# Performance work log

Hardware: AMD Instinct MI355X
Metric: run time of the kernel (lower is better)

Reference implementation:

```python
import jax, jax.numpy as jnp
import numpy as np

D = 1024        # embedding_dim
H = 16          # num_heads
HKV = 4         # num_kv_heads
HD = D // H     # head_dim = 64
L = 64          # latent_dim
EPS = 1e-6
LN_EPS = 1e-5
B, S = 2, 1024


def _feat(x):
    # feature_map == 'elu': elu(x) + 1 (non-negative features)
    return jax.nn.elu(x) + 1.0


def setup_inputs() -> dict:
    key = jax.random.key(0)
    ks = jax.random.split(key, 8)
    w = lambda k, shape: (jax.random.normal(k, shape, jnp.float32) * 0.02)
    return {
        "x": jax.random.normal(ks[0], (B, S, D), jnp.float32),
        "Wq": w(ks[1], (D, D)), "bq": jnp.zeros((D,), jnp.float32),
        "Wk": w(ks[2], (D, HKV * HD)), "bk": jnp.zeros((HKV * HD,), jnp.float32),
        "Wv": w(ks[3], (D, HKV * HD)), "bv": jnp.zeros((HKV * HD,), jnp.float32),
        "Wc": w(ks[4], (HKV * HD, L)),   # kv_compress (no bias)
        "We": w(ks[5], (L, HKV * HD)),   # kv_expand (no bias)
        "Wo": w(ks[6], (D, D)), "bo": jnp.zeros((D,), jnp.float32),
        "gamma": jnp.ones((D,), jnp.float32),
        "beta": jnp.zeros((D,), jnp.float32),
    }


def reference(x, Wq, bq, Wk, bk, Wv, bv, Wc, We, Wo, bo, gamma, beta):
    b, s, _ = x.shape
    residual = x
    # projections
    q = x @ Wq + bq                     # [b,s,D]
    k = x @ Wk + bk                     # [b,s,HKV*HD]
    v = x @ Wv + bv
    # latent compress -> expand
    k = (k @ Wc) @ We                   # [b,s,HKV*HD]
    v = (v @ Wc) @ We
    # split heads
    q = q.reshape(b, s, H, HD).transpose(0, 2, 1, 3)      # [b,H,s,HD]
    k = k.reshape(b, s, HKV, HD).transpose(0, 2, 1, 3)    # [b,HKV,s,HD]
    v = v.reshape(b, s, HKV, HD).transpose(0, 2, 1, 3)
    # GQA: repeat KV heads per query group
    rep = H // HKV
    k = jnp.repeat(k, rep, axis=1)                        # [b,H,s,HD]
    v = jnp.repeat(v, rep, axis=1)
    # causal linear attention via cumulative KV outer-product state
    qf = _feat(q)                                          # [b,h,s,f]
    kf = _feat(k)
    kv = jnp.einsum('bhsf,bhsd->bhsfd', kf, v)             # [b,h,s,f,d]
    kv_cum = jnp.cumsum(kv, axis=2)
    num = jnp.einsum('bhsf,bhsfd->bhsd', qf, kv_cum)
    den = jnp.einsum('bhsf,bhsf->bhs', qf, jnp.cumsum(kf, axis=2))[..., None] + EPS
    o = num / den                                          # [b,h,s,d]
    # merge heads, output projection
    o = o.transpose(0, 2, 1, 3).reshape(b, s, D)
    o = o @ Wo + bo
    # residual + layernorm (epsilon=1e-5)
    y = residual + o
    mu = jnp.mean(y, axis=-1, keepdims=True)
    var = jnp.var(y, axis=-1, keepdims=True)
    return (y - mu) / jnp.sqrt(var + LN_EPS) * gamma + beta
```

## Files before the change

kernel.cpp:

```cpp
#include <hip/hip_runtime.h>

#define D_ 1024
#define H_ 16
#define HKV_ 4
#define B_ 2
#define S_ 1024
#define BS_ (B_*S_)
#define QKVW 1536
#define QB 64
#define NC (S_/QB)

typedef short bf8 __attribute__((ext_vector_type(8)));
typedef float f32x4 __attribute__((ext_vector_type(4)));

#define MFMA_B16(a,b,c) __builtin_amdgcn_mfma_f32_16x16x32_bf16((a),(b),(c),0,0,0)

#define GLOAD16(g, l) __builtin_amdgcn_global_load_lds( \
    (const __attribute__((address_space(1))) void*)(g), \
    (__attribute__((address_space(3))) void*)(l), 16, 0, 0)

#define SW(row, idx) ((idx) ^ (((row) & 7) << 3))

__device__ __forceinline__ unsigned short f2b(float f) {
  unsigned int u = __float_as_uint(f);
  u += 0x7FFFu + ((u >> 16) & 1u);
  return (unsigned short)(u >> 16);
}
__device__ __forceinline__ float b2f(unsigned short h) {
  return __uint_as_float(((unsigned int)h) << 16);
}
__device__ __forceinline__ float feat(float x) { return x > 0.f ? x + 1.f : __expf(x); }

__device__ __forceinline__ void conv_body(const float* __restrict__ src,
                                          unsigned short* __restrict__ dst,
                                          int sub, int n4, int tid) {
  int i = sub * 256 + tid;
  if (i >= n4) return;
  float4 v = ((const float4*)src)[i];
  ushort4 o;
  o.x = f2b(v.x); o.y = f2b(v.y); o.z = f2b(v.z); o.w = f2b(v.w);
  ((ushort4*)dst)[i] = o;
}

__device__ __forceinline__ void tconv_body(const float* __restrict__ src,
                                           unsigned short* __restrict__ dst,
                                           int bx, int by, int ss, int ds,
                                           int tid, float (*tl)[65]) {
  int r0 = by * 64, c0 = bx * 64;
  int ty = tid >> 4, tx4 = (tid & 15) * 4;
#pragma unroll
  for (int rep = 0; rep < 4; ++rep) {
    int r = ty + rep * 16;
    float4 v = *(const float4*)&src[(size_t)(r0 + r) * ss + c0 + tx4];
    tl[r][tx4] = v.x; tl[r][tx4 + 1] = v.y; tl[r][tx4 + 2] = v.z; tl[r][tx4 + 3] = v.w;
  }
  __syncthreads();
#pragma unroll
  for (int rep = 0; rep < 4; ++rep) {
    int c = ty + rep * 16;
    ushort4 o;
    o.x = f2b(tl[tx4 + 0][c]); o.y = f2b(tl[tx4 + 1][c]);
    o.z = f2b(tl[tx4 + 2][c]); o.w = f2b(tl[tx4 + 3][c]);
    *(ushort4*)&dst[(size_t)(c0 + c) * ds + r0 + tx4] = o;
  }
}

__global__ __launch_bounds__(256) void k_prep(const float* __restrict__ x,
                                              const float* __restrict__ Wq,
                                              const float* __restrict__ Wo,
                                              const float* __restrict__ Wk,
                                              const float* __restrict__ Wv,
                                              const float* __restrict__ Wc,
                                              const float* __restrict__ We,
                                              const float* __restrict__ bq,
                                              const float* __restrict__ bk,
                                              const float* __restrict__ bv,
                                              unsigned short* __restrict__ xb,
                                              unsigned short* __restrict__ Wqkv_t,
                                              unsigned short* __restrict__ Wo_t,
                                              float* __restrict__ biasq) {
  __shared__ __align__(16) unsigned char smem[46080];
  int blk = blockIdx.x, tid = threadIdx.x;
  if (blk < 2048) {
    conv_body(x, xb, blk, BS_ * D_ / 4, tid);
  } else if (blk < 2304) {
    int sb = blk - 2048;
    tconv_body(Wq, Wqkv_t, sb & 15, sb >> 4, 1024, 1024, tid, (float(*)[65])smem);
  } else if (blk < 2560) {
    int sb = blk - 2304;
    tconv_body(Wo, Wo_t, sb & 15, sb >> 4, 1024, 1024, tid, (float(*)[65])smem);
  } else if (blk < 2624) {
    int sb = blk - 2560;
    int bx = sb & 15, by = sb >> 4;
    int col0 = bx * 128, row0 = by * 64;
    unsigned short (*Aw)[72] = (unsigned short(*)[72])smem;
    unsigned short (*Bc)[72] = (unsigned short(*)[72])(smem + 64 * 72 * 2);
    {
      int j = tid >> 2, c4 = (tid & 3) * 16;
      const float* src = &We[(size_t)j * 256 + row0 + c4];
#pragma unroll
      for (int e = 0; e < 16; e += 4) {
        float4 v = *(const float4*)(src + e);
        Aw[c4 + e + 0][j] = f2b(v.x); Aw[c4 + e + 1][j] = f2b(v.y);
        Aw[c4 + e + 2][j] = f2b(v.z); Aw[c4 + e + 3][j] = f2b(v.w);
      }
      const float* wsrc = &Wc[(size_t)tid * 64];
#pragma unroll
      for (int e = 0; e < 64; e += 4) {
        float4 v = *(const float4*)(wsrc + e);
        Bc[tid][e + 0] = f2b(v.x); Bc[tid][e + 1] = f2b(v.y);
        Bc[tid][e + 2] = f2b(v.z); Bc[tid][e + 3] = f2b(v.w);
      }
    }
    __syncthreads();
    const int lane = tid & 63, wave = tid >> 6;
    const int lr = lane & 15, lq = lane >> 4;
    const f32x4 fzero = {0.f, 0.f, 0.f, 0.f};
    f32x4 tacc[4][4];
#pragma unroll
    for (int i = 0; i < 4; ++i)
#pragma unroll
      for (int j = 0; j < 4; ++j) tacc[i][j] = fzero;
#pragma unroll
    for (int kk = 0; kk < 2; ++kk)
#pragma unroll
      for (int mi = 0; mi < 4; ++mi) {
        bf8 a = *(const bf8*)&Aw[mi * 16 + lr][kk * 32 + lq * 8];
#pragma unroll
        for (int ni = 0; ni < 4; ++ni) {
          bf8 bb = *(const bf8*)&Bc[wave * 64 + ni * 16 + lr][kk * 32 + lq * 8];
          tacc[mi][ni] = MFMA_B16(a, bb, tacc[mi][ni]);
        }
      }
    __syncthreads();
    unsigned short (*T)[264] = (unsigned short(*)[264])smem;
#pragma unroll
    for (int mi = 0; mi < 4; ++mi)
#pragma unroll
      for (int ni = 0; ni < 4; ++ni) {
        int k = wave * 64 + ni * 16 + lr;
#pragma unroll
        for (int r = 0; r < 4; ++r)
          T[mi * 16 + lq * 4 + r][k] = f2b(tacc[mi][ni][r]);
      }
    __syncthreads();
    unsigned short (*Bs)[40] = (unsigned short(*)[40])(smem + 64 * 264 * 2);
    f32x4 acc2[4][2];
#pragma unroll
    for (int i = 0; i < 4; ++i) { acc2[i][0] = fzero; acc2[i][1] = fzero; }
    for (int k0 = 0; k0 < 256; k0 += 32) {
      {
        int colr = tid >> 1, half = tid & 1;
        int col = col0 + colr;
        const float* src = (col < 1024)
            ? &Wk[(size_t)col * 256 + k0 + half * 16]
            : &Wv[(size_t)(col - 1024) * 256 + k0 + half * 16];
#pragma unroll
        for (int e = 0; e < 16; e += 4) {
          float4 v = *(const float4*)(src + e);
          Bs[colr][half * 16 + e + 0] = f2b(v.x);
          Bs[colr][half * 16 + e + 1] = f2b(v.y);
          Bs[colr][half * 16 + e + 2] = f2b(v.z);
          Bs[colr][half * 16 + e + 3] = f2b(v.w);
        }
      }
      __syncthreads();
#pragma unroll
      for (int mi = 0; mi < 4; ++mi) {
        bf8 a = *(const bf8*)&T[mi * 16 + lr][k0 + lq * 8];
#pragma unroll
        for (int ni = 0; ni < 2; ++ni) {
          bf8 bb = *(const bf8*)&Bs[wave * 32 + ni * 16 + lr][lq * 8];
          acc2[mi][ni] = MFMA_B16(a, bb, acc2[mi][ni]);
        }
      }
      __syncthreads();
    }
#pragma unroll
    for (int mi = 0; mi < 4; ++mi)
#pragma unroll
      for (int ni = 0; ni < 2; ++ni) {
        int col = col0 + wave * 32 + ni * 16 + lr;
        int sec = col >> 10, cc = col & 1023;
#pragma unroll
        for (int r = 0; r < 4; ++r) {
          int row = row0 + mi * 16 + lq * 4 + r;
          Wqkv_t[(size_t)(1024 + sec * 256 + row) * 1024 + cc] = f2b(acc2[mi][ni][r]);
        }
      }
  } else if (blk == 2624) {
    float* tb = (float*)smem;
    if (tid < 128) {
      int l = tid & 63;
      const float* bsrc = (tid < 64) ? bk : bv;
      float s = 0.f;
      for (int j = 0; j < 256; ++j) s += bsrc[j] * Wc[(size_t)j * 64 + l];
      tb[tid] = s;
    }
    __syncthreads();
    {
      float s0 = 0.f, s1 = 0.f;
      for (int l = 0; l < 64; ++l) {
        float w = We[(size_t)l * 256 + tid];
        s0 += tb[l] * w;
        s1 += tb[64 + l] * w;
      }
      biasq[1024 + tid] = s0;
      biasq[1280 + tid] = s1;
    }
  } else {
    ((float4*)biasq)[tid] = ((const float4*)bq)[tid];
  }
}

template<int MODE>
__global__ __launch_bounds__(64) void k_gemm1(const unsigned short* __restrict__ A,
                                              const unsigned short* __restrict__ Bt,
                                              const float* __restrict__ bias,
                                              unsigned short* __restrict__ C,
                                              int N, int K) {
  __shared__ __align__(16) unsigned short As[2][64 * 64];
  __shared__ __align__(16) unsigned short Bs[2][64 * 64];
  const int lane = threadIdx.x;
  const int row0 = blockIdx.y * 64, col0 = blockIdx.x * 64;
  const int lr = lane & 15, lq = lane >> 4;
  const int rsub = lane >> 3, sj = lane & 7;
  const int js = sj ^ rsub;
  const f32x4 fzero = {0.f, 0.f, 0.f, 0.f};
  f32x4 acc[4][4];
#pragma unroll
  for (int i = 0; i < 4; ++i)
#pragma unroll
    for (int j = 0; j < 4; ++j) acc[i][j] = fzero;

#define STAGE64(pb, k0)                                                        \
  {                                                                            \
    _Pragma("unroll")                                                          \
    for (int i = 0; i < 8; ++i)                                                \
      GLOAD16(&A[(size_t)(row0 + i * 8 + rsub) * K + (k0) + js * 8],           \
              &As[pb][(i * 512 + lane * 8)]);                                  \
    _Pragma("unroll")                                                          \
    for (int i = 0; i < 8; ++i)                                                \
      GLOAD16(&Bt[(size_t)(col0 + i * 8 + rsub) * K + (k0) + js * 8],          \
              &Bs[pb][(i * 512 + lane * 8)]);                                  \
  }

  STAGE64(0, 0);
  int cur = 0;
  for (int k0 = 0; k0 < K; k0 += 64) {
    if (k0 + 64 < K) {
      STAGE64(cur ^ 1, k0 + 64);
      asm volatile("s_waitcnt vmcnt(16)" ::: "memory");
    } else {
      asm volatile("s_waitcnt vmcnt(0)" ::: "memory");
    }
    __builtin_amdgcn_sched_barrier(0);
    bf8 af[2][4], bfr[2][4];
#pragma unroll
    for (int kk = 0; kk < 2; ++kk)
#pragma unroll
      for (int mi = 0; mi < 4; ++mi) {
        int ch = (kk * 4 + lq) ^ (lr & 7);
        af[kk][mi]  = *(const bf8*)&As[cur][(mi * 16 + lr) * 64 + ch * 8];
        bfr[kk][mi] = *(const bf8*)&Bs[cur][(mi * 16 + lr) * 64 + ch * 8];
      }
#pragma unroll
    for (int kk = 0; kk < 2; ++kk)
#pragma unroll
      for (int mi = 0; mi < 4; ++mi)
#pragma unroll
        for (int ni = 0; ni < 4; ++ni)
          acc[mi][ni] = MFMA_B16(af[kk][mi], bfr[kk][ni], acc[mi][ni]);
    cur ^= 1;
  }
#undef STAGE64
#pragma unroll
  for (int ni = 0; ni < 4; ++ni) {
    int col = col0 + ni * 16 + lr;
    float bv = bias[col];
#pragma unroll
    for (int mi = 0; mi < 4; ++mi)
#pragma unroll
      for (int r = 0; r < 4; ++r) {
        int row = row0 + mi * 16 + lq * 4 + r;
        float v = acc[mi][ni][r] + bv;
        if (MODE == 1 && col < 1280) v = feat(v);
        C[(size_t)row * N + col] = f2b(v);
      }
  }
}

__global__ __launch_bounds__(256) void k_vkv(const unsigned short* __restrict__ qkvb,
                                             float* __restrict__ stc) {
  __shared__ unsigned short tl[64][72];
  __shared__ float Kf[64 * 64];
  int c = blockIdx.x, g = blockIdx.y, b = blockIdx.z;
  int tid = threadIdx.x;
  int s0 = c * QB;
  {
    int j = tid >> 2, f0 = (tid & 3) * 16;
    const unsigned short* kr = &qkvb[(size_t)(b * S_ + s0 + j) * QKVW + 1024 + g * 64 + f0];
    const unsigned short* vr = &qkvb[(size_t)(b * S_ + s0 + j) * QKVW + 1280 + g * 64 + f0];
    uint4 k0_ = *(const uint4*)kr;
    uint4 k1_ = *(const uint4*)(kr + 8);
    const unsigned short* ks = (const unsigned short*)&k0_;
#pragma unroll
    for (int e = 0; e < 8; ++e) Kf[j * 64 + f0 + e] = b2f(ks[e]);
    ks = (const unsigned short*)&k1_;
#pragma unroll
    for (int e = 0; e < 8; ++e) Kf[j * 64 + f0 + 8 + e] = b2f(ks[e]);
    *(uint4*)&tl[j][f0] = *(const uint4*)vr;
    *(uint4*)&tl[j][f0 + 8] = *(const uint4*)(vr + 8);
  }
  __syncthreads();
  int d = tid >> 2, f0 = (tid & 3) * 16;
  float acc[16];
#pragma unroll
  for (int e = 0; e < 16; ++e) acc[e] = 0.f;
#pragma unroll 4
  for (int j = 0; j < QB; ++j) {
    float vv = b2f(tl[j][d]);
    const float* kfr = &Kf[j * 64 + f0];
#pragma unroll
    for (int e = 0; e < 16; ++e) acc[e] += vv * kfr[e];
  }
  size_t base = ((size_t)((b * HKV_ + g) * NC + c) * 65 + d) * 64 + f0;
#pragma unroll
  for (int e = 0; e < 16; ++e) stc[base + e] = acc[e];
  if (tid < 64) {
    float z = 0.f;
    for (int j = 0; j < QB; ++j) z += Kf[j * 64 + tid];
    stc[((size_t)((b * HKV_ + g) * NC + c) * 65 + 64) * 64 + tid] = z;
  }
}

__global__ __launch_bounds__(512) void k_attn(const unsigned short* __restrict__ qkvb,
                                              const float* __restrict__ stc,
                                              unsigned short* __restrict__ ob) {
  __shared__ __align__(16) unsigned short Kf[64 * 64];
  __shared__ __align__(16) unsigned short Vl[64 * 64];
  __shared__ __align__(16) unsigned short Sl[64 * 64];
  __shared__ __align__(16) unsigned short P[2][64 * 64];
  __shared__ float zl[64];
  __shared__ float qz[2][64];
  __shared__ float den[2][64];
  int c = blockIdx.x, hp = blockIdx.y, b = blockIdx.z;
  int g = hp >> 1;
  int tid = threadIdx.x, lane = tid & 63, wave = tid >> 6;
  int s0 = c * QB;
  const int lr = lane & 15, lq = lane >> 4, lk = lq * 8;
  const int hh = wave >> 2, rw = (wave & 3) * 16;
  unsigned short* Pv = &P[0][0];

  {
    int t = tid & 255;
    int j = t >> 2, f0 = (t & 3) * 16;
    if (tid < 256) {
      const unsigned short* kr =
          &qkvb[(size_t)(b * S_ + s0 + j) * QKVW + 1024 + g * 64 + f0];
      *(uint4*)&Kf[SW(j, j * 64 + f0)]     = *(const uint4*)kr;
      *(uint4*)&Kf[SW(j, j * 64 + f0 + 8)] = *(const uint4*)(kr + 8);
    } else {
      const unsigned short* vr =
          &qkvb[(size_t)(b * S_ + s0 + j) * QKVW + 1280 + g * 64 + f0];
      *(uint4*)&Pv[j * 72 + f0]     = *(const uint4*)vr;
      *(uint4*)&Pv[j * 72 + f0 + 8] = *(const uint4*)(vr + 8);
    }
  }
  {
    int dd = tid >> 3, col = (tid & 7) * 8;
    const float* sb = stc + (size_t)(b * HKV_ + g) * NC * 4160 + dd * 64 + col;
    float p0[8], p1[8], p2[8], p3[8];
#pragma unroll
    for (int e = 0; e < 8; ++e) { p0[e] = 0.f; p1[e] = 0.f; p2[e] = 0.f; p3[e] = 0.f; }
    int cc = 0;
    for (; cc + 4 <= c; cc += 4) {
      const float* q0 = sb + (size_t)(cc + 0) * 4160;
      const float* q1 = sb + (size_t)(cc + 1) * 4160;
      const float* q2 = sb + (size_t)(cc + 2) * 4160;
      const float* q3 = sb + (size_t)(cc + 3) * 4160;
      float4 a0 = *(const float4*)q0, b0 = *(const float4*)(q0 + 4);
      float4 a1 = *(const float4*)q1, b1 = *(const float4*)(q1 + 4);
      float4 a2 = *(const float4*)q2, b2 = *(const float4*)(q2 + 4);
      float4 a3 = *(const float4*)q3, b3 = *(const float4*)(q3 + 4);
      p0[0] += a0.x; p0[1] += a0.y; p0[2] += a0.z; p0[3] += a0.w;
      p0[4] += b0.x; p0[5] += b0.y; p0[6] += b0.z; p0[7] += b0.w;
      p1[0] += a1.x; p1[1] += a1.y; p1[2] += a1.z; p1[3] += a1.w;
      p1[4] += b1.x; p1[5] += b1.y; p1[6] += b1.z; p1[7] += b1.w;
      p2[0] += a2.x; p2[1] += a2.y; p2[2] += a2.z; p2[3] += a2.w;
      p2[4] += b2.x; p2[5] += b2.y; p2[6] += b2.z; p2[7] += b2.w;
      p3[0] += a3.x; p3[1] += a3.y; p3[2] += a3.z; p3[3] += a3.w;
      p3[4] += b3.x; p3[5] += b3.y; p3[6] += b3.z; p3[7] += b3.w;
    }
    for (; cc < c; ++cc) {
      const float* q0 = sb + (size_t)cc * 4160;
      float4 a0 = *(const float4*)q0, b0 = *(const float4*)(q0 + 4);
      p0[0] += a0.x; p0[1] += a0.y; p0[2] += a0.z; p0[3] += a0.w;
      p0[4] += b0.x; p0[5] += b0.y; p0[6] += b0.z; p0[7] += b0.w;
    }
    unsigned short o[8];
#pragma unroll
    for (int e = 0; e < 8; ++e) o[e] = f2b(p0[e] + p1[e] + p2[e] + p3[e]);
    *(uint4*)&Sl[SW(dd, dd * 64 + col)] = *(const uint4*)o;
    if (tid < 64) {
      const float* zb = stc + (size_t)(b * HKV_ + g) * NC * 4160 + 64 * 64 + tid;
      float z0 = 0.f, z1 = 0.f, z2 = 0.f, z3 = 0.f;
      int c2 = 0;
      for (; c2 + 4 <= c; c2 += 4) {
        z0 += zb[(size_t)(c2 + 0) * 4160];
        z1 += zb[(size_t)(c2 + 1) * 4160];
        z2 += zb[(size_t)(c2 + 2) * 4160];
        z3 += zb[(size_t)(c2 + 3) * 4160];
      }
      for (; c2 < c; ++c2) z0 += zb[(size_t)c2 * 4160];
      zl[tid] = z0 + z1 + z2 + z3;
    }
  }
  bf8 aQ[2];
  {
    const unsigned short* qr =
        &qkvb[(size_t)(b * S_ + s0 + rw + lr) * QKVW + (hp * 2 + hh) * 64];
    aQ[0] = *(const bf8*)(qr + lk);
    aQ[1] = *(const bf8*)(qr + 32 + lk);
  }
  __syncthreads();
  {
    int d = tid >> 3, sq = (tid & 7) * 8;
    unsigned short tmp[8];
#pragma unroll
    for (int e = 0; e < 8; ++e) tmp[e] = Pv[(sq + e) * 72 + d];
    *(uint4*)&Vl[SW(d, d * 64 + sq)] = *(const uint4*)tmp;
  }
  {
    float qdot = 0.f;
#pragma unroll
    for (int kk = 0; kk < 2; ++kk)
#pragma unroll
      for (int e = 0; e < 8; ++e)
        qdot += b2f((unsigned short)aQ[kk][e]) * zl[kk * 32 + lq * 8 + e];
    qdot += __shfl_xor(qdot, 16);
    qdot += __shfl_xor(qdot, 32);
    if (lq == 0) qz[hh][rw + lr] = qdot;
  }
  __syncthreads();
  const f32x4 fzero = {0.f, 0.f, 0.f, 0.f};
  f32x4 sc[4];
#pragma unroll
  for (int nj = 0; nj < 4; ++nj) sc[nj] = fzero;
#pragma unroll
  for (int nj = 0; nj < 4; ++nj)
#pragma unroll
    for (int kk = 0; kk < 2; ++kk) {
      bf8 bk8 = *(const bf8*)&Kf[SW(nj * 16 + lr, (nj * 16 + lr) * 64 + kk * 32 + lk)];
      sc[nj] = MFMA_B16(aQ[kk], bk8, sc[nj]);
    }
#pragma unroll
  for (int nj = 0; nj < 4; ++nj)
#pragma unroll
    for (int r = 0; r < 4; ++r) {
      int i = rw + lq * 4 + r;
      int j = nj * 16 + lr;
      float v = (j <= i) ? sc[nj][r] : 0.f;
      P[hh][SW(i, i * 64 + j)] = f2b(v);
    }
  __syncthreads();
  {
    int hd = tid >> 8, t = tid & 255;
    int i = t >> 2, q = t & 3, f0 = q * 16;
    float s = 0.f;
#pragma unroll
    for (int e = 0; e < 16; ++e) s += b2f(P[hd][SW(i, i * 64 + f0 + e)]);
    s += __shfl_xor(s, 1);
    s += __shfl_xor(s, 2);
    if (q == 0) den[hd][i] = s + qz[hd][i];
  }
  f32x4 oa[4];
#pragma unroll
  for (int nd = 0; nd < 4; ++nd) oa[nd] = fzero;
  bf8 aP[2];
#pragma unroll
  for (int kk = 0; kk < 2; ++kk)
    aP[kk] = *(const bf8*)&P[hh][SW(rw + lr, (rw + lr) * 64 + kk * 32 + lk)];
#pragma unroll
  for (int nd = 0; nd < 4; ++nd)
#pragma unroll
    for (int kk = 0; kk < 2; ++kk) {
      bf8 bS = *(const bf8*)&Sl[SW(nd * 16 + lr, (nd * 16 + lr) * 64 + kk * 32 + lk)];
      oa[nd] = MFMA_B16(aQ[kk], bS, oa[nd]);
      bf8 bV = *(const bf8*)&Vl[SW(nd * 16 + lr, (nd * 16 + lr) * 64 + kk * 32 + lk)];
      oa[nd] = MFMA_B16(aP[kk], bV, oa[nd]);
    }
  __syncthreads();
#pragma unroll
  for (int nd = 0; nd < 4; ++nd)
#pragma unroll
    for (int r = 0; r < 4; ++r) {
      int i = rw + lq * 4 + r;
      int dd = nd * 16 + lr;
      (&P[0][0])[i * 128 + hh * 64 + dd] = f2b(oa[nd][r] / (den[hh][i] + 1e-6f));
    }
  __syncthreads();
  {
    int j = tid >> 3, u = tid & 7;
    unsigned short* orow = &ob[(size_t)(b * S_ + s0 + j) * D_ + hp * 128 + u * 16];
    *(uint4*)orow       = *(const uint4*)&(&P[0][0])[j * 128 + u * 16];
    *(uint4*)(orow + 8) = *(const uint4*)&(&P[0][0])[j * 128 + u * 16 + 8];
  }
}

__global__ __launch_bounds__(256) void k_ln(const unsigned short* __restrict__ xb,
                                            const unsigned short* __restrict__ o2,
                                            const float* __restrict__ gamma,
                                            const float* __restrict__ beta,
                                            float* __restrict__ out) {
  int row = blockIdx.x, tid = threadIdx.x;
  ushort4 xv = ((const ushort4*)(xb + (size_t)row * D_))[tid];
  ushort4 ov = ((const ushort4*)(o2 + (size_t)row * D_))[tid];
  float4 y;
  y.x = b2f(xv.x) + b2f(ov.x); y.y = b2f(xv.y) + b2f(ov.y);
  y.z = b2f(xv.z) + b2f(ov.z); y.w = b2f(xv.w) + b2f(ov.w);
  float s = y.x + y.y + y.z + y.w;
  float ss = y.x * y.x + y.y * y.y + y.z * y.z + y.w * y.w;
#pragma unroll
  for (int off = 32; off > 0; off >>= 1) {
    s += __shfl_down(s, off);
    ss += __shfl_down(ss, off);
  }
  __shared__ float red[8];
  int lane = tid & 63, wave = tid >> 6;
  if (lane == 0) { red[wave] = s; red[4 + wave] = ss; }
  __syncthreads();
  if (tid == 0) {
    red[0] = red[0] + red[1] + red[2] + red[3];
    red[4] = red[4] + red[5] + red[6] + red[7];
  }
  __syncthreads();
  float mu = red[0] * (1.f / D_);
  float var = red[4] * (1.f / D_) - mu * mu;
  float rs = rsqrtf(var + 1e-5f);
  float4 g4 = ((const float4*)gamma)[tid];
  float4 b4 = ((const float4*)beta)[tid];
  float4 o;
  o.x = (y.x - mu) * rs * g4.x + b4.x;
  o.y = (y.y - mu) * rs * g4.y + b4.y;
  o.z = (y.z - mu) * rs * g4.z + b4.z;
  o.w = (y.w - mu) * rs * g4.w + b4.w;
  ((float4*)(out + (size_t)row * D_))[tid] = o;
}

extern "C" void kernel_launch(void* const* d_in, const int* in_sizes, int n_in,
                              void* d_out, int out_size, void* d_ws, size_t ws_size,
                              hipStream_t stream) {
  const float* x     = (const float*)d_in[0];
  const float* Wq    = (const float*)d_in[1];
  const float* bq    = (const float*)d_in[2];
  const float* Wk    = (const float*)d_in[3];
  const float* bk    = (const float*)d_in[4];
  const float* Wv    = (const float*)d_in[5];
  const float* bv    = (const float*)d_in[6];
  const float* Wc    = (const float*)d_in[7];
  const float* We    = (const float*)d_in[8];
  const float* Wo    = (const float*)d_in[9];
  const float* bo    = (const float*)d_in[10];
  const float* gamma = (const float*)d_in[11];
  const float* beta  = (const float*)d_in[12];

  char* p = (char*)d_ws;
  size_t off = 0;
  auto carve = [&](size_t bytes) {
    void* r = p + off;
    off = (off + bytes + 255) & ~(size_t)255;
    return r;
  };
  unsigned short* xb     = (unsigned short*)carve((size_t)BS_ * D_ * 2);
  unsigned short* Wqkv_t = (unsigned short*)carve((size_t)QKVW * D_ * 2);
  unsigned short* Wo_t   = (unsigned short*)carve((size_t)D_ * D_ * 2);
  float*          biasq  = (float*)carve(QKVW * 4);
  unsigned short* qkvb   = (unsigned short*)carve((size_t)BS_ * QKVW * 2);
  float*          stc    = (float*)carve((size_t)8 * NC * 65 * 64 * 4);
  unsigned short* obuf   = (unsigned short*)carve((size_t)BS_ * D_ * 2);
  unsigned short* o2     = (unsigned short*)carve((size_t)BS_ * D_ * 2);

  k_prep<<<2626, 256, 0, stream>>>(x, Wq, Wo, Wk, Wv, Wc, We, bq, bk, bv,
                                   xb, Wqkv_t, Wo_t, biasq);
  k_gemm1<1><<<dim3(24, 32), 64, 0, stream>>>(xb, Wqkv_t, biasq, qkvb, QKVW, 1024);
  k_vkv<<<dim3(NC, HKV_, B_), 256, 0, stream>>>(qkvb, stc);
  k_attn<<<dim3(NC, H_ / 2, B_), 512, 0, stream>>>(qkvb, stc, obuf);
  k_gemm1<0><<<dim3(16, 32), 64, 0, stream>>>(obuf, Wo_t, bo, o2, 1024, 1024);
  k_ln<<<BS_, 256, 0, stream>>>(xb, o2, gamma, beta, (float*)d_out);
}
```

Baseline: 81.44 us.

## Fuse chunk-state and attention kernels with atomic flag handoff

Merges the per-chunk KV state kernel and the attention kernel into one launch of 384 blocks. The first 128 blocks compute chunk states and signal completion per (batch, kv-group) through release atomics, and the attention blocks spin on those flags before reading the states. Q fragments and K/V tiles are loaded before the wait so they overlap with it. This removes one kernel launch and the gap between the two kernels, but it relies on producer blocks being scheduled before or alongside the spinning consumers, and it adds a flag reset inside the prep kernel.

New measurement: 123.1 us. 51.2% more time.

```diff
diff --git a/kernel.cpp b/kernel.cpp
--- a/kernel.cpp
+++ b/kernel.cpp
@@ -78,7 +78,8 @@
                                               unsigned short* __restrict__ xb,
                                               unsigned short* __restrict__ Wqkv_t,
                                               unsigned short* __restrict__ Wo_t,
-                                              float* __restrict__ biasq) {
+                                              float* __restrict__ biasq,
+                                              int* __restrict__ flags) {
   __shared__ __align__(16) unsigned char smem[46080];
   int blk = blockIdx.x, tid = threadIdx.x;
   if (blk < 2048) {
@@ -210,6 +211,7 @@
     }
   } else {
     ((float4*)biasq)[tid] = ((const float4*)bq)[tid];
+    if (tid < 8) flags[tid] = 0;
   }
 }
 
@@ -290,67 +292,77 @@
   }
 }
 
-__global__ __launch_bounds__(256) void k_vkv(const unsigned short* __restrict__ qkvb,
-                                             float* __restrict__ stc) {
-  __shared__ unsigned short tl[64][72];
-  __shared__ float Kf[64 * 64];
-  int c = blockIdx.x, g = blockIdx.y, b = blockIdx.z;
-  int tid = threadIdx.x;
+__global__ __launch_bounds__(512) void k_va(const unsigned short* __restrict__ qkvb,
+                                            float* __restrict__ stc,
+                                            unsigned short* __restrict__ ob,
+                                            int* __restrict__ flags) {
+  __shared__ __align__(16) unsigned char smem[42496];
+  int bid = blockIdx.x, tid = threadIdx.x;
+
+  if (bid < 128) {
+    int c = bid & 15, g = (bid >> 4) & 3, b = bid >> 6;
+    int s0 = c * QB;
+    unsigned short (*tl)[72] = (unsigned short(*)[72])smem;
+    float* Kff = (float*)(smem + 16384);
+    {
+      int j = tid >> 3, f0 = (tid & 7) * 8;
+      const unsigned short* kr = &qkvb[(size_t)(b * S_ + s0 + j) * QKVW + 1024 + g * 64 + f0];
+      const unsigned short* vr = &qkvb[(size_t)(b * S_ + s0 + j) * QKVW + 1280 + g * 64 + f0];
+      uint4 kv = *(const uint4*)kr;
+      const unsigned short* ks = (const unsigned short*)&kv;
+#pragma unroll
+      for (int e = 0; e < 8; ++e) Kff[j * 64 + f0 + e] = b2f(ks[e]);
+      *(uint4*)&tl[j][f0] = *(const uint4*)vr;
+    }
+    __syncthreads();
+    int d = tid >> 3, f0 = (tid & 7) * 8;
+    float acc[8];
+#pragma unroll
+    for (int e = 0; e < 8; ++e) acc[e] = 0.f;
+#pragma unroll 4
+    for (int j = 0; j < QB; ++j) {
+      float vv = b2f(tl[j][d]);
+      const float* kfr = &Kff[j * 64 + f0];
+#pragma unroll
+      for (int e = 0; e < 8; ++e) acc[e] += vv * kfr[e];
+    }
+    {
+      size_t base = ((size_t)((b * HKV_ + g) * NC + c) * 65 + d) * 64 + f0;
+      float4 o0 = {acc[0], acc[1], acc[2], acc[3]};
+      float4 o1 = {acc[4], acc[5], acc[6], acc[7]};
+      *(float4*)&stc[base] = o0;
+      *(float4*)&stc[base + 4] = o1;
+    }
+    if (tid < 64) {
+      float z = 0.f;
+      for (int j = 0; j < QB; ++j) z += Kff[j * 64 + tid];
+      stc[((size_t)((b * HKV_ + g) * NC + c) * 65 + 64) * 64 + tid] = z;
+    }
+    __syncthreads();
+    __threadfence();
+    if (tid == 0)
+      __hip_atomic_fetch_add(&flags[b * HKV_ + g], 1,
+                             __ATOMIC_RELEASE, __HIP_MEMORY_SCOPE_AGENT);
+    return;
+  }
+
+  int a = bid - 128;
+  int c = a & 15, hp = (a >> 4) & 7, b = a >> 7;
+  int g = hp >> 1;
   int s0 = c * QB;
-  {
-    int j = tid >> 2, f0 = (tid & 3) * 16;
-    const unsigned short* kr = &qkvb[(size_t)(b * S_ + s0 + j) * QKVW + 1024 + g * 64 + f0];
-    const unsigned short* vr = &qkvb[(size_t)(b * S_ + s0 + j) * QKVW + 1280 + g * 64 + f0];
-    uint4 k0_ = *(const uint4*)kr;
-    uint4 k1_ = *(const uint4*)(kr + 8);
-    const unsigned short* ks = (const unsigned short*)&k0_;
-#pragma unroll
-    for (int e = 0; e < 8; ++e) Kf[j * 64 + f0 + e] = b2f(ks[e]);
-    ks = (const unsigned short*)&k1_;
-#pragma unroll
-    for (int e = 0; e < 8; ++e) Kf[j * 64 + f0 + 8 + e] = b2f(ks[e]);
-    *(uint4*)&tl[j][f0] = *(const uint4*)vr;
-    *(uint4*)&tl[j][f0 + 8] = *(const uint4*)(vr + 8);
-  }
-  __syncthreads();
-  int d = tid >> 2, f0 = (tid & 3) * 16;
-  float acc[16];
-#pragma unroll
-  for (int e = 0; e < 16; ++e) acc[e] = 0.f;
-#pragma unroll 4
-  for (int j = 0; j < QB; ++j) {
-    float vv = b2f(tl[j][d]);
-    const float* kfr = &Kf[j * 64 + f0];
-#pragma unroll
-    for (int e = 0; e < 16; ++e) acc[e] += vv * kfr[e];
-  }
-  size_t base = ((size_t)((b * HKV_ + g) * NC + c) * 65 + d) * 64 + f0;
-#pragma unroll
-  for (int e = 0; e < 16; ++e) stc[base + e] = acc[e];
-  if (tid < 64) {
-    float z = 0.f;
-    for (int j = 0; j < QB; ++j) z += Kf[j * 64 + tid];
-    stc[((size_t)((b * HKV_ + g) * NC + c) * 65 + 64) * 64 + tid] = z;
-  }
-}
-
-__global__ __launch_bounds__(512) void k_attn(const unsigned short* __restrict__ qkvb,
-                                              const float* __restrict__ stc,
-                                              unsigned short* __restrict__ ob) {
-  __shared__ __align__(16) unsigned short Kf[64 * 64];
-  __shared__ __align__(16) unsigned short Vl[64 * 64];
-  __shared__ __align__(16) unsigned short Sl[64 * 64];
-  __shared__ __align__(16) unsigned short P[2][64 * 64];
-  __shared__ float zl[64];
-  __shared__ float qz[2][64];
-  __shared__ float den[2][64];
-  int c = blockIdx.x, hp = blockIdx.y, b = blockIdx.z;
-  int g = hp >> 1;
-  int tid = threadIdx.x, lane = tid & 63, wave = tid >> 6;
-  int s0 = c * QB;
+  const int lane = tid & 63, wave = tid >> 6;
   const int lr = lane & 15, lq = lane >> 4, lk = lq * 8;
   const int hh = wave >> 2, rw = (wave & 3) * 16;
-  unsigned short* Pv = &P[0][0];
+  unsigned short* Kf = (unsigned short*)smem;
+  unsigned short* Vl = (unsigned short*)(smem + 8192);
+  unsigned short* Sl = (unsigned short*)(smem + 16384);
+  unsigned short* P0 = (unsigned short*)(smem + 24576);
+  unsigned short* P1 = (unsigned short*)(smem + 32768);
+  float* zl  = (float*)(smem + 40960);
+  float* qz  = (float*)(smem + 41216);
+  float* den = (float*)(smem + 41728);
+  unsigned short* Pv = P0;
+  unsigned short* Ph = hh ? P1 : P0;
 
   {
     int t = tid & 255;
@@ -367,6 +379,19 @@
       *(uint4*)&Pv[j * 72 + f0 + 8] = *(const uint4*)(vr + 8);
     }
   }
+  bf8 aQ[2];
+  {
+    const unsigned short* qr =
+        &qkvb[(size_t)(b * S_ + s0 + rw + lr) * QKVW + (hp * 2 + hh) * 64];
+    aQ[0] = *(const bf8*)(qr + lk);
+    aQ[1] = *(const bf8*)(qr + 32 + lk);
+  }
+  if (tid == 0) {
+    while (__hip_atomic_load(&flags[b * HKV_ + g],
+                             __ATOMIC_ACQUIRE, __HIP_MEMORY_SCOPE_AGENT) < NC)
+      __builtin_amdgcn_s_sleep(2);
+  }
+  __syncthreads();
   {
     int dd = tid >> 3, col = (tid & 7) * 8;
     const float* sb = stc + (size_t)(b * HKV_ + g) * NC * 4160 + dd * 64 + col;
@@ -416,14 +441,6 @@
       zl[tid] = z0 + z1 + z2 + z3;
     }
   }
-  bf8 aQ[2];
-  {
-    const unsigned short* qr =
-        &qkvb[(size_t)(b * S_ + s0 + rw + lr) * QKVW + (hp * 2 + hh) * 64];
-    aQ[0] = *(const bf8*)(qr + lk);
-    aQ[1] = *(const bf8*)(qr + 32 + lk);
-  }
-  __syncthreads();
   {
     int d = tid >> 3, sq = (tid & 7) * 8;
     unsigned short tmp[8];
@@ -431,6 +448,7 @@
     for (int e = 0; e < 8; ++e) tmp[e] = Pv[(sq + e) * 72 + d];
     *(uint4*)&Vl[SW(d, d * 64 + sq)] = *(const uint4*)tmp;
   }
+  __syncthreads();
   {
     float qdot = 0.f;
 #pragma unroll
@@ -440,9 +458,8 @@
         qdot += b2f((unsigned short)aQ[kk][e]) * zl[kk * 32 + lq * 8 + e];
     qdot += __shfl_xor(qdot, 16);
     qdot += __shfl_xor(qdot, 32);
-    if (lq == 0) qz[hh][rw + lr] = qdot;
-  }
-  __syncthreads();
+    if (lq == 0) qz[hh * 64 + rw + lr] = qdot;
+  }
   const f32x4 fzero = {0.f, 0.f, 0.f, 0.f};
   f32x4 sc[4];
 #pragma unroll
@@ -461,18 +478,19 @@
       int i = rw + lq * 4 + r;
       int j = nj * 16 + lr;
       float v = (j <= i) ? sc[nj][r] : 0.f;
-      P[hh][SW(i, i * 64 + j)] = f2b(v);
+      Ph[SW(i, i * 64 + j)] = f2b(v);
     }
   __syncthreads();
   {
     int hd = tid >> 8, t = tid & 255;
     int i = t >> 2, q = t & 3, f0 = q * 16;
+    unsigned short* Pd = hd ? P1 : P0;
     float s = 0.f;
 #pragma unroll
-    for (int e = 0; e < 16; ++e) s += b2f(P[hd][SW(i, i * 64 + f0 + e)]);
+    for (int e = 0; e < 16; ++e) s += b2f(Pd[SW(i, i * 64 + f0 + e)]);
     s += __shfl_xor(s, 1);
     s += __shfl_xor(s, 2);
-    if (q == 0) den[hd][i] = s + qz[hd][i];
+    if (q == 0) den[hd * 64 + i] = s + qz[hd * 64 + i];
   }
   f32x4 oa[4];
 #pragma unroll
@@ -480,7 +498,7 @@
   bf8 aP[2];
 #pragma unroll
   for (int kk = 0; kk < 2; ++kk)
-    aP[kk] = *(const bf8*)&P[hh][SW(rw + lr, (rw + lr) * 64 + kk * 32 + lk)];
+    aP[kk] = *(const bf8*)&Ph[SW(rw + lr, (rw + lr) * 64 + kk * 32 + lk)];
 #pragma unroll
   for (int nd = 0; nd < 4; ++nd)
 #pragma unroll
@@ -497,14 +515,14 @@
     for (int r = 0; r < 4; ++r) {
       int i = rw + lq * 4 + r;
       int dd = nd * 16 + lr;
-      (&P[0][0])[i * 128 + hh * 64 + dd] = f2b(oa[nd][r] / (den[hh][i] + 1e-6f));
+      P0[i * 128 + hh * 64 + dd] = f2b(oa[nd][r] / (den[hh * 64 + i] + 1e-6f));
     }
   __syncthreads();
   {
     int j = tid >> 3, u = tid & 7;
     unsigned short* orow = &ob[(size_t)(b * S_ + s0 + j) * D_ + hp * 128 + u * 16];
-    *(uint4*)orow       = *(const uint4*)&(&P[0][0])[j * 128 + u * 16];
-    *(uint4*)(orow + 8) = *(const uint4*)&(&P[0][0])[j * 128 + u * 16 + 8];
+    *(uint4*)orow       = *(const uint4*)&P0[j * 128 + u * 16];
+    *(uint4*)(orow + 8) = *(const uint4*)&P0[j * 128 + u * 16 + 8];
   }
 }
 
@@ -580,12 +598,12 @@
   float*          stc    = (float*)carve((size_t)8 * NC * 65 * 64 * 4);
   unsigned short* obuf   = (unsigned short*)carve((size_t)BS_ * D_ * 2);
   unsigned short* o2     = (unsigned short*)carve((size_t)BS_ * D_ * 2);
+  int*            flags  = (int*)carve(256);
 
   k_prep<<<2626, 256, 0, stream>>>(x, Wq, Wo, Wk, Wv, Wc, We, bq, bk, bv,
-                                   xb, Wqkv_t, Wo_t, biasq);
+                                   xb, Wqkv_t, Wo_t, biasq, flags);
   k_gemm1<1><<<dim3(24, 32), 64, 0, stream>>>(xb, Wqkv_t, biasq, qkvb, QKVW, 1024);
-  k_vkv<<<dim3(NC, HKV_, B_), 256, 0, stream>>>(qkvb, stc);
-  k_attn<<<dim3(NC, H_ / 2, B_), 512, 0, stream>>>(qkvb, stc, obuf);
+  k_va<<<384, 512, 0, stream>>>(qkvb, stc, obuf, flags);
   k_gemm1<0><<<dim3(16, 32), 64, 0, stream>>>(obuf, Wo_t, bo, o2, 1024, 1024);
   k_ln<<<BS_, 256, 0, stream>>>(xb, o2, gamma, beta, (float*)d_out);
 }
```
